# Performance work log

Measured on AMD Instinct MI355X. Metric: run time of the kernel, lower is better.

The kernel has to match this reference:

```python
import jax, jax.numpy as jnp
import numpy as np

B, T, N, PRED, DM = 16, 512, 128, 256, 32
L = T + PRED  # 768; conv windows 12 then 4: 768 -> 64 -> 16
EPS = 1e-5


def _conv1d(x, w, b, stride):
    # x: [B, C, L'], w: [C, C, k], kernel_size == stride, VALID (matches torch Conv1d)
    out = jax.lax.conv_general_dilated(x, w, (stride,), 'VALID',
                                       dimension_numbers=('NCH', 'OIH', 'NCH'))
    return out + b[None, :, None]


def _conv2d(x, w, b, pad):
    out = jax.lax.conv_general_dilated(x, w, (1, 1), [(pad, pad), (pad, pad)],
                                       dimension_numbers=('NCHW', 'OIHW', 'NCHW'))
    return out + b[None, :, None, None]


def _bn1d(x, g, b):
    # BatchNorm1d, training-mode batch statistics over (batch, length) per channel
    mu = x.mean((0, 2), keepdims=True)
    var = ((x - mu) ** 2).mean((0, 2), keepdims=True)
    return (x - mu) * jax.lax.rsqrt(var + EPS) * g[None, :, None] + b[None, :, None]


def _cubic_spline(y, size):
    # Natural cubic spline through values y: [B, Lk, C] at knots t = linspace(0,1,Lk),
    # evaluated at linspace(0,1,size). Natural BC: second derivative M=0 at endpoints.
    Bb, Lk, C = y.shape
    h = 1.0 / (Lk - 1)
    # tridiagonal system for interior second derivatives (uniform knots):
    # M[i-1] + 4 M[i] + M[i+1] = 6 * (y[i+1] - 2 y[i] + y[i-1]) / h^2
    m = Lk - 2
    rhs = (y[:, 2:, :] - 2.0 * y[:, 1:-1, :] + y[:, :-2, :]) * (6.0 / (h * h))  # [B,m,C]
    A = 4.0 * jnp.eye(m, dtype=y.dtype) + jnp.eye(m, k=1, dtype=y.dtype) + jnp.eye(m, k=-1, dtype=y.dtype)
    Mi = jnp.linalg.solve(A, rhs.transpose(1, 0, 2).reshape(m, Bb * C))  # [m, B*C]
    Mi = Mi.reshape(m, Bb, C).transpose(1, 0, 2)
    M = jnp.pad(Mi, ((0, 0), (1, 1), (0, 0)))  # [B, Lk, C], M[0]=M[-1]=0
    q = jnp.linspace(0.0, 1.0, size).astype(y.dtype)
    idx = jnp.clip(jnp.floor(q * (Lk - 1)).astype(jnp.int32), 0, Lk - 2)  # [size]
    s = (q - idx.astype(y.dtype) * h)[None, :, None]  # offset within interval
    u = h - s
    yi, yi1 = y[:, idx, :], y[:, idx + 1, :]
    M0, M1 = M[:, idx, :], M[:, idx + 1, :]
    hh6 = h * h / 6.0
    return ((M0 * u ** 3 + M1 * s ** 3) / (6.0 * h)
            + (yi - M0 * hh6) * (u / h)
            + (yi1 - M1 * hh6) * (s / h))  # [B, size, C]


def _forward(batch_x, le_w, le_b, c1_w, c1_b, bn1_g, bn1_b, c2_w, c2_b, bn2_g, bn2_b,
             i1_w0, i1_b0, i1_w1, i1_b1, i2_w0, i2_b0, i2_w1, i2_b1, ld_w, ld_b):
    # instance norm over time
    means = batch_x.mean(1, keepdims=True)
    xc = batch_x - means
    stdev = jnp.sqrt(xc.var(axis=1, keepdims=True) + EPS)
    xn = xc / stdev                               # [B, T, N]
    x = xn.transpose(0, 2, 1)                     # [B, N, T]
    x = jnp.einsum('bnt,lt->bnl', x, le_w) + le_b  # length_encoder -> [B, N, L]
    # multi-scale downsampling conv + spline back up to L
    scales = []
    t = x
    for win, cw, cb, g, bb in ((12, c1_w, c1_b, bn1_g, bn1_b), (4, c2_w, c2_b, bn2_g, bn2_b)):
        t = jax.nn.elu(_bn1d(_conv1d(t, cw, cb, win), g, bb))      # [B, N, L//...]
        scales.append(_cubic_spline(t.transpose(0, 2, 1), L).transpose(0, 2, 1))  # [B, N, L]
    a = jnp.stack([x] + scales, axis=1).transpose(0, 1, 3, 2)  # [B, 3, L, N]
    # Inception block 1 (num_kernels=2: 1x1 and 3x3, averaged), Dropout(eval)=id, GELU(exact)
    h1 = 0.5 * (_conv2d(a, i1_w0, i1_b0, 0) + _conv2d(a, i1_w1, i1_b1, 1))  # [B, DM, L, N]
    h1 = jax.nn.gelu(h1, approximate=False)
    # Inception block 2 -> 1 channel
    h2 = 0.5 * (_conv2d(h1, i2_w0, i2_b0, 0) + _conv2d(h1, i2_w1, i2_b1, 1))  # [B, 1, L, N]
    co = x + h2[:, 0].transpose(0, 2, 1)          # residual, [B, N, L]
    f = jnp.einsum('bnl,pl->bnp', co, ld_w) + ld_b  # length_decoder -> [B, N, PRED]
    f = f.transpose(0, 2, 1)                      # [B, PRED, N]
    return f * stdev[:, 0, :][:, None, :] + means[:, 0, :][:, None, :]


def setup_inputs():
    key = jax.random.key(0)
    ks = jax.random.split(key, 20)
    def w(i, shape, scale=0.02):
        return scale * jax.random.normal(ks[i], shape, jnp.float32)
    return dict(
        batch_x=jax.random.normal(ks[0], (B, T, N), jnp.float32),
        batch_x_mark=jax.random.normal(ks[1], (B, T, 4), jnp.float32),
        dec_inp=jax.random.normal(ks[2], (B, PRED, N), jnp.float32),
        batch_y_mark=jax.random.normal(ks[3], (B, PRED, 4), jnp.float32),
        le_w=w(4, (L, T)), le_b=w(5, (L,)),
        c1_w=w(6, (N, N, 12)), c1_b=w(7, (N,)),
        bn1_g=jnp.ones((N,), jnp.float32), bn1_b=jnp.zeros((N,), jnp.float32),
        c2_w=w(8, (N, N, 4)), c2_b=w(9, (N,)),
        bn2_g=jnp.ones((N,), jnp.float32), bn2_b=jnp.zeros((N,), jnp.float32),
        i1_w0=w(10, (DM, 3, 1, 1), 0.1), i1_b0=jnp.zeros((DM,), jnp.float32),
        i1_w1=w(11, (DM, 3, 3, 3), 0.1), i1_b1=jnp.zeros((DM,), jnp.float32),
        i2_w0=w(12, (1, DM, 1, 1), 0.1), i2_b0=jnp.zeros((1,), jnp.float32),
        i2_w1=w(13, (1, DM, 3, 3), 0.1), i2_b1=jnp.zeros((1,), jnp.float32),
        ld_w=w(14, (PRED, L)), ld_b=w(15, (PRED,)),
    )


def reference(batch_x, batch_x_mark, dec_inp, batch_y_mark, le_w, le_b,
              c1_w, c1_b, bn1_g, bn1_b, c2_w, c2_b, bn2_g, bn2_b,
              i1_w0, i1_b0, i1_w1, i1_b1, i2_w0, i2_b0, i2_w1, i2_b1, ld_w, ld_b):
    # batch_x_mark / dec_inp / batch_y_mark are accepted but unused (as in the torch forward)
    return _forward(batch_x, le_w, le_b, c1_w, c1_b, bn1_g, bn1_b, c2_w, c2_b, bn2_g, bn2_b,
                    i1_w0, i1_b0, i1_w1, i1_b1, i2_w0, i2_b0, i2_w1, i2_b1, ld_w, ld_b)
```

## Files before the change

### kernel.cpp

```cpp
#include <hip/hip_runtime.h>
#include <hip/hip_bf16.h>
#include <math.h>

#define BB 16
#define TT 512
#define NN 128
#define PREDN 256
#define DMC 32
#define LL 768
constexpr float EPSF = 1e-5f;
using bf16 = __hip_bfloat16;
using frag_ab = __attribute__((ext_vector_type(8))) short;
using frag_cd = __attribute__((ext_vector_type(4))) float;

__device__ __forceinline__ unsigned pbf2(float a, float b){
  union { bf16 h; unsigned short u; } x, y;
  x.h = __float2bfloat16(a); y.h = __float2bfloat16(b);
  return (unsigned)x.u | ((unsigned)y.u << 16);
}

__device__ __forceinline__ unsigned short bf16b(float v){
  union { bf16 h; unsigned short u; } x;
  x.h = __float2bfloat16(v);
  return x.u;
}

__device__ __forceinline__ float gelu_fast(float s){
  float s2v = s*s;
  float e = exp2f(s*fmaf(s2v, 0.10294396f, 2.30211806f));
  return s*e*__builtin_amdgcn_rcpf(e + 1.f);
}

__global__ void k_pre(const float* __restrict__ bx, const float* __restrict__ v0,
                      const float* __restrict__ v1, const float* __restrict__ w1c,
                      const float* __restrict__ w2c, float* __restrict__ sp,
                      float* __restrict__ s2p, float* __restrict__ vwsT,
                      float* __restrict__ wT1, float* __restrict__ wT2){
  int blk = blockIdx.x;
  if(blk < 64){
    int b = blk >> 2, tq = blk & 3, n = threadIdx.x;
    const float* p = bx + (size_t)b*TT*NN + (size_t)tq*128*NN + n;
    float s = 0.f, s2 = 0.f;
    for(int t=0;t<128;t++){ float v = p[(size_t)t*NN]; s += v; s2 += v*v; }
    sp[tq*2048 + b*NN + n] = s;
    s2p[tq*2048 + b*NN + n] = s2;
  } else if(blk == 64){
    for(int i=threadIdx.x; i<9*DMC; i+=blockDim.x){
      int tap = i/DMC, c = i%DMC;
      float wv = 0.5f*v1[c*9 + tap];
      if(tap == 4) wv += 0.5f*v0[c];
      vwsT[i] = wv;
    }
  } else if(blk <= 192){
    int o = blk - 65;
    for(int k=threadIdx.x; k<1536; k+=blockDim.x)
      wT1[(size_t)k*NN + o] = w1c[(size_t)o*1536 + k];
  } else {
    int o = blk - 193;
    for(int k=threadIdx.x; k<512; k+=blockDim.x)
      wT2[(size_t)k*NN + o] = w2c[(size_t)o*512 + k];
  }
}

__global__ __launch_bounds__(256) void k_gemm1(const float* __restrict__ bx, const float* __restrict__ lew,
    const float* __restrict__ leb, const float* __restrict__ sp, const float* __restrict__ s2p,
    float* __restrict__ x, float* __restrict__ a0){
  __shared__ unsigned Asu[64*20];
  __shared__ unsigned Bsu[64*20];
  int tid = threadIdx.x;
  int row0 = blockIdx.x*64, l0 = blockIdx.y*64;
  int b = row0 >> 7, n0 = row0 & 127;
  int lane = tid & 63, wv = tid >> 6;
  frag_cd acc[4] = {};
  int an = tid & 63, akq = (tid >> 6)*8;
  float mu_a, rs_a;
  {
    int rowa = row0 + an;
    float ssum = 0.f, s2sum = 0.f;
    #pragma unroll
    for(int tq=0;tq<4;tq++){ ssum += sp[tq*2048 + rowa]; s2sum += s2p[tq*2048 + rowa]; }
    mu_a = ssum*(1.f/512.f);
    rs_a = 1.f/sqrtf(fmaxf(s2sum*(1.f/512.f) - mu_a*mu_a, 0.f) + EPSF);
  }
  int btk = tid & 15, blc = tid >> 4;
  unsigned ra[4], rbq[4];
  #pragma unroll
  for(int u=0;u<4;u++){
    float v0 = (bx[((size_t)b*TT + akq + 2*u)*NN + n0 + an] - mu_a)*rs_a;
    float v1 = (bx[((size_t)b*TT + akq + 2*u + 1)*NN + n0 + an] - mu_a)*rs_a;
    ra[u] = pbf2(v0, v1);
    const float* lp = lew + (size_t)(l0 + blc + 16*u)*TT + 2*btk;
    rbq[u] = pbf2(lp[0], lp[1]);
  }
  int fr = wv*16 + (lane & 15);
  int fq = (lane >> 4)*4;
  for(int k0=0;k0<TT;k0+=32){
    *(uint4*)&Asu[an*20 + (akq>>1)] = make_uint4(ra[0], ra[1], ra[2], ra[3]);
    #pragma unroll
    for(int p=0;p<4;p++) Bsu[(blc + 16*p)*20 + btk] = rbq[p];
    __syncthreads();
    if(k0 + 32 < TT){
      #pragma unroll
      for(int u=0;u<4;u++){
        float v0 = (bx[((size_t)b*TT + k0 + 32 + akq + 2*u)*NN + n0 + an] - mu_a)*rs_a;
        float v1 = (bx[((size_t)b*TT + k0 + 32 + akq + 2*u + 1)*NN + n0 + an] - mu_a)*rs_a;
        ra[u] = pbf2(v0, v1);
        const float* lp = lew + (size_t)(l0 + blc + 16*u)*TT + k0 + 32 + 2*btk;
        rbq[u] = pbf2(lp[0], lp[1]);
      }
    }
    frag_ab af = *(const frag_ab*)&Asu[fr*20 + fq];
    #pragma unroll
    for(int nt=0;nt<4;nt++){
      frag_ab bf = *(const frag_ab*)&Bsu[(nt*16 + (lane & 15))*20 + fq];
      acc[nt] = __builtin_amdgcn_mfma_f32_16x16x32_bf16(af, bf, acc[nt], 0, 0, 0);
    }
    __syncthreads();
  }
  int col = lane & 15, quad = lane >> 4;
  #pragma unroll
  for(int nt=0;nt<4;nt++){
    int l = l0 + nt*16 + col;
    float lb = leb[l];
    #pragma unroll
    for(int r=0;r<4;r++){
      int m = wv*16 + quad*4 + r;
      x[(size_t)(row0 + m)*LL + l] = acc[nt][r] + lb;
    }
    float4 st;
    st.x = acc[nt][0] + lb;
    st.y = acc[nt][1] + lb;
    st.z = acc[nt][2] + lb;
    st.w = acc[nt][3] + lb;
    *(float4*)&a0[((size_t)b*LL + l)*NN + n0 + wv*16 + quad*4] = st;
  }
}

__global__ __launch_bounds__(512) void k_conv1(const float* __restrict__ x, const float* __restrict__ wT,
                                               const float* __restrict__ bias, float* __restrict__ t1){
  __shared__ alignas(16) float xs[NN*48];
  int jt = blockIdx.x, b = blockIdx.y;
  int tid = threadIdx.x;
  int o = tid & 127, jj = tid >> 7;
  for(int i=tid;i<NN*48;i+=512){
    int ci = i/48, kk = i%48;
    xs[i] = x[((size_t)b*NN + ci)*LL + jt*48 + kk];
  }
  __syncthreads();
  float a0 = 0.f, a1 = 0.f, a2 = 0.f, a3 = 0.f;
  for(int ci=0;ci<NN;ci++){
    const float* xc = xs + ci*48 + jj*12;
    const float* wc = wT + (size_t)(ci*12)*NN + o;
    #pragma unroll
    for(int kk=0;kk<12;kk+=4){
      a0 = fmaf(xc[kk+0], wc[(size_t)(kk+0)*NN], a0);
      a1 = fmaf(xc[kk+1], wc[(size_t)(kk+1)*NN], a1);
      a2 = fmaf(xc[kk+2], wc[(size_t)(kk+2)*NN], a2);
      a3 = fmaf(xc[kk+3], wc[(size_t)(kk+3)*NN], a3);
    }
  }
  int j = jt*4 + jj;
  t1[((size_t)b*NN + o)*64 + j] = (a0 + a1) + (a2 + a3) + bias[o];
}

__global__ void k_bnstats(const float* __restrict__ t, const float* __restrict__ g, const float* __restrict__ bb,
                          int Bcnt, int Jcnt, float* __restrict__ scale, float* __restrict__ shift){
  int o = blockIdx.x;
  int tot = Bcnt*Jcnt;
  float s = 0.f, s2 = 0.f;
  for(int i=threadIdx.x; i<tot; i+=blockDim.x){
    int b = i / Jcnt, j = i % Jcnt;
    float v = t[((size_t)b*NN + o)*Jcnt + j];
    s += v; s2 += v*v;
  }
  __shared__ float rs[256], rs2[256];
  rs[threadIdx.x] = s; rs2[threadIdx.x] = s2;
  __syncthreads();
  for(int st=128; st>0; st>>=1){
    if(threadIdx.x < st){ rs[threadIdx.x] += rs[threadIdx.x+st]; rs2[threadIdx.x] += rs2[threadIdx.x+st]; }
    __syncthreads();
  }
  if(threadIdx.x == 0){
    float mu = rs[0]/tot;
    float var = fmaxf(rs2[0]/tot - mu*mu, 0.f);
    float sc = g[o] * rsqrtf(var + EPSF);
    scale[o] = sc; shift[o] = bb[o] - mu*sc;
  }
}

__global__ void k_bnelu_t(const float* __restrict__ t, const float* __restrict__ scale,
                          const float* __restrict__ shift, int Jcnt, float* __restrict__ tt){
  int j = blockIdx.x, b = blockIdx.y, o = threadIdx.x;
  float v = t[((size_t)b*NN + o)*Jcnt + j]*scale[o] + shift[o];
  v = v > 0.f ? v : (expf(v) - 1.f);
  tt[((size_t)b*Jcnt + j)*NN + o] = v;
}

template<int LK>
__global__ void k_spline_solve(const float* __restrict__ y, float* __restrict__ M){
  constexpr int m = LK-2;
  const float Kc = 6.f*(LK-1)*(LK-1);
  __shared__ float cp[m];
  __shared__ float dp[m][NN];
  int b = blockIdx.x, c = threadIdx.x;
  if(c == 0){
    float cv = 0.25f; cp[0] = cv;
    for(int i=1;i<m;i++){ cv = 1.f/(4.f - cv); cp[i] = cv; }
  }
  __syncthreads();
  const float* yb = y + (size_t)b*LK*NN + c;
  float y0 = yb[0], y1 = yb[NN];
  float dprev = 0.f;
  for(int i=0;i<m;i++){
    float y2 = yb[(size_t)(i+2)*NN];
    float r = (y2 - 2.f*y1 + y0)*Kc;
    float d = (i == 0) ? r*0.25f : (r - dprev)*cp[i];
    dp[i][c] = d; dprev = d;
    y0 = y1; y1 = y2;
  }
  float* Mb = M + (size_t)b*LK*NN + c;
  float xv = dp[m-1][c];
  Mb[(size_t)m*NN] = xv;
  for(int i=m-2;i>=0;i--){
    xv = dp[i][c] - cp[i]*xv;
    Mb[(size_t)(i+1)*NN] = xv;
  }
  Mb[0] = 0.f;
  Mb[(size_t)(LK-1)*NN] = 0.f;
}

__device__ __forceinline__ float spline_pt(const float* __restrict__ y, const float* __restrict__ M,
                                           int LK, int l, int b, int c){
  float hh = 1.f/(LK-1);
  float q = (float)l * (1.f/(LL-1));
  int idx = (int)floorf(q*(LK-1));
  if(idx > LK-2) idx = LK-2;
  float s = q - idx*hh;
  float u = hh - s;
  const float* yb = y + ((size_t)b*LK + idx)*NN + c;
  const float* Mb = M + ((size_t)b*LK + idx)*NN + c;
  float yi = yb[0], yi1 = yb[NN], M0 = Mb[0], M1 = Mb[NN];
  float hh6 = hh*hh/6.f;
  return (M0*u*u*u + M1*s*s*s)*(1.f/(6.f*hh))
       + (yi  - M0*hh6)*(u*(1.f/hh))
       + (yi1 - M1*hh6)*(s*(1.f/hh));
}

__global__ __launch_bounds__(512) void k_conv2(const float* __restrict__ tt, const float* __restrict__ wT,
                                               const float* __restrict__ bias, float* __restrict__ t2){
  __shared__ alignas(16) float ts[16*NN];
  int jt = blockIdx.x, b = blockIdx.y;
  int tid = threadIdx.x;
  int o = tid & 127, jj = tid >> 7;
  for(int i=tid;i<16*NN;i+=512)
    ts[i] = tt[((size_t)b*64 + jt*16)*NN + i];
  __syncthreads();
  float a0 = 0.f, a1 = 0.f, a2 = 0.f, a3 = 0.f;
  for(int ci=0;ci<NN;ci++){
    const float* wc = wT + (size_t)(ci*4)*NN + o;
    const float* tc2 = ts + (jj*4)*NN + ci;
    a0 = fmaf(tc2[0*NN], wc[0*NN], a0);
    a1 = fmaf(tc2[1*NN], wc[1*NN], a1);
    a2 = fmaf(tc2[2*NN], wc[2*NN], a2);
    a3 = fmaf(tc2[3*NN], wc[3*NN], a3);
  }
  int j = jt*4 + jj;
  t2[((size_t)b*NN + o)*16 + j] = (a0 + a1) + (a2 + a3) + bias[o];
}

constexpr int KOFF[27] = {
    0,   1,   2,  36,  37,  38,  72,  73,  74,
  432, 433, 434, 468, 469, 470, 504, 505, 506,
  864, 865, 866, 900, 901, 902, 936, 937, 938
};

#define PBQ 1416
__global__ __launch_bounds__(256, 5) void k_h12(const float* __restrict__ a0,
    const float* __restrict__ y64, const float* __restrict__ M64,
    const float* __restrict__ y16, const float* __restrict__ M16,
    const float* __restrict__ w0, const float* __restrict__ b0,
    const float* __restrict__ w1, const float* __restrict__ b1,
    const float* __restrict__ vwsT, const float* __restrict__ vb0,
    const float* __restrict__ vb1, float* __restrict__ co){
  constexpr int AR = 12, AC = 36;
  __shared__ alignas(16) float as[3][AR][AC];
  __shared__ alignas(16) unsigned Au[4*PBQ];
  int tid = threadIdx.x;
  int l0 = blockIdx.x*8, n0 = blockIdx.y*32, b = blockIdx.z;
  int lane = tid & 63, wv = tid >> 6;

  float* asf = &as[0][0][0];
  for(int i=tid; i<3*AR*AC; i+=256){
    int ch = i/(AR*AC), rem = i%(AR*AC), yy = rem/AC, xx = rem%AC;
    int gl = l0 + yy - 2, gn = n0 + xx - 2;
    float v = 0.f;
    if(gl >= 0 && gl < LL && gn >= 0 && gn < NN){
      if(ch == 0)      v = a0[((size_t)b*LL + gl)*NN + gn];
      else if(ch == 1) v = spline_pt(y64, M64, 64, gl, b, gn);
      else             v = spline_pt(y16, M16, 16, gl, b, gn);
    }
    asf[i] = v;
  }

  int colB = lane & 15, kq = (lane >> 4)*8;
  union { uint4 q; frag_ab f; } bw0, bw1;
  {
    float w8[2][8];
    #pragma unroll
    for(int nt=0;nt<2;nt++){
      #pragma unroll
      for(int j=0;j<8;j++){
        int k = kq + j;
        float w = 0.f;
        if(k < 27){
          int ci = k/9, r9 = k - ci*9, dy = r9/3, dx = r9 - dy*3;
          int c = nt*16 + colB;
          w = 0.5f*w1[((c*3+ci)*3+dy)*3+dx];
          if(dy==1 && dx==1) w += 0.5f*w0[c*3+ci];
        }
        w8[nt][j] = w;
      }
    }
    bw0.q = make_uint4(pbf2(w8[0][0],w8[0][1]), pbf2(w8[0][2],w8[0][3]),
                       pbf2(w8[0][4],w8[0][5]), pbf2(w8[0][6],w8[0][7]));
    bw1.q = make_uint4(pbf2(w8[1][0],w8[1][1]), pbf2(w8[1][2],w8[1][3]),
                       pbf2(w8[1][4],w8[1][5]), pbf2(w8[1][6],w8[1][7]));
  }
  float br0 = 0.5f*(b0[colB] + b1[colB]);
  float br1 = 0.5f*(b0[16 + colB] + b1[16 + colB]);
  __syncthreads();

  for(int base=0; base<352; base+=128){
    int px = base + (tid >> 1);
    int half = tid & 1;
    if(px < 352){
      uint4 oA, oB;
      if(px < 340){
        int yy = px/34, xx = px - yy*34;
        const float* bp = asf + yy*AC + xx;
        if(half == 0){
          oA.x = pbf2(bp[KOFF[0]],  bp[KOFF[1]]);
          oA.y = pbf2(bp[KOFF[2]],  bp[KOFF[3]]);
          oA.z = pbf2(bp[KOFF[4]],  bp[KOFF[5]]);
          oA.w = pbf2(bp[KOFF[6]],  bp[KOFF[7]]);
          oB.x = pbf2(bp[KOFF[8]],  bp[KOFF[9]]);
          oB.y = pbf2(bp[KOFF[10]], bp[KOFF[11]]);
          oB.z = pbf2(bp[KOFF[12]], bp[KOFF[13]]);
          oB.w = pbf2(bp[KOFF[14]], bp[KOFF[15]]);
        } else {
          oA.x = pbf2(bp[KOFF[16]], bp[KOFF[17]]);
          oA.y = pbf2(bp[KOFF[18]], bp[KOFF[19]]);
          oA.z = pbf2(bp[KOFF[20]], bp[KOFF[21]]);
          oA.w = pbf2(bp[KOFF[22]], bp[KOFF[23]]);
          oB.x = pbf2(bp[KOFF[24]], bp[KOFF[25]]);
          oB.y = pbf2(bp[KOFF[26]], 0.f);
          oB.z = 0u; oB.w = 0u;
        }
      } else {
        oA = make_uint4(0u,0u,0u,0u);
        oB = make_uint4(0u,0u,0u,0u);
      }
      *(uint4*)&Au[(2*half)*PBQ + px*4]     = oA;
      *(uint4*)&Au[(2*half+1)*PBQ + px*4]   = oB;
    }
  }
  __syncthreads();

  unsigned short* h1h = (unsigned short*)Au;
  frag_cd zac = {0.f, 0.f, 0.f, 0.f};
  int qg = lane >> 4;
  int g0 = colB >> 3, s0 = colB & 7;
  for(int t = wv; t < 22; t += 4){
    int arow = t*16 + colB;
    union { uint4 q; frag_ab f; } av;
    av.q = *(const uint4*)&Au[qg*PBQ + arow*4];
    frag_cd d0 = __builtin_amdgcn_mfma_f32_16x16x32_bf16(av.f, bw0.f, zac, 0, 0, 0);
    frag_cd d1 = __builtin_amdgcn_mfma_f32_16x16x32_bf16(av.f, bw1.f, zac, 0, 0, 0);
    int px0 = t*16 + qg*4;
    #pragma unroll
    for(int r=0;r<4;r++){
      int px = px0 + r;
      h1h[(g0*PBQ + px*4)*2 + s0]     = bf16b(gelu_fast(d0[r] + br0));
      h1h[((g0+2)*PBQ + px*4)*2 + s0] = bf16b(gelu_fast(d1[r] + br1));
    }
  }
  __syncthreads();

  if(n0 == 0){
    for(int i=tid;i<10*32;i+=256){ int yy=i>>5, ch=i&31;
      h1h[((ch>>3)*PBQ + (yy*34)*4)*2 + (ch&7)] = 0; }
  }
  if(n0 == 96){
    for(int i=tid;i<10*32;i+=256){ int yy=i>>5, ch=i&31;
      h1h[((ch>>3)*PBQ + (yy*34+33)*4)*2 + (ch&7)] = 0; }
  }
  if(l0 == 0){
    for(int i=tid;i<34*32;i+=256){ int xx=i>>5, ch=i&31;
      h1h[((ch>>3)*PBQ + xx*4)*2 + (ch&7)] = 0; }
  }
  if(l0 == 760){
    for(int i=tid;i<34*32;i+=256){ int xx=i>>5, ch=i&31;
      h1h[((ch>>3)*PBQ + (9*34+xx)*4)*2 + (ch&7)] = 0; }
  }

  union { uint4 q; frag_ab f; } aw[9];
  {
    bool wlane = (lane & 15) == 0;
    int c8 = qg*8;
    #pragma unroll
    for(int tap=0; tap<9; tap++){
      const float* wp = vwsT + tap*DMC + c8;
      float4 wa = *(const float4*)wp;
      float4 wb = *(const float4*)(wp+4);
      if(!wlane){ wa = make_float4(0.f,0.f,0.f,0.f); wb = make_float4(0.f,0.f,0.f,0.f); }
      aw[tap].q = make_uint4(pbf2(wa.x,wa.y), pbf2(wa.z,wa.w), pbf2(wb.x,wb.y), pbf2(wb.z,wb.w));
    }
  }
  float vbsum = vb0[0] + vb1[0];
  __syncthreads();

  frag_cd cacc[4] = {};
  int baseoff[4];
  #pragma unroll
  for(int tt=0; tt<4; tt++){
    int px = (wv*4 + tt)*16 + (lane & 15);
    int yy = px >> 5, xx = px & 31;
    baseoff[tt] = qg*PBQ + (yy*34 + xx)*4;
  }
  #pragma unroll
  for(int dy=0; dy<3; dy++)
    #pragma unroll
    for(int dx=0; dx<3; dx++){
      int tap = dy*3 + dx;
      int off = (dy*34 + dx)*4;
      #pragma unroll
      for(int tt=0; tt<4; tt++){
        union { uint4 q; frag_ab f; } bv;
        bv.q = *(const uint4*)&Au[baseoff[tt] + off];
        cacc[tt] = __builtin_amdgcn_mfma_f32_16x16x32_bf16(aw[tap].f, bv.f, cacc[tt], 0, 0, 0);
      }
    }
  if(lane < 16){
    #pragma unroll
    for(int tt=0; tt<4; tt++){
      int px = (wv*4 + tt)*16 + lane;
      int yy = px >> 5, xx = px & 31;
      float res = as[0][yy+2][xx+2];
      size_t idx = ((size_t)b*LL + l0 + yy)*NN + n0 + xx;
      co[idx] = cacc[tt][0] + vbsum + res;
    }
  }
}

__global__ __launch_bounds__(256) void k_gemm2(const float* __restrict__ a0, const float* __restrict__ ldw,
    const float* __restrict__ ldb, const float* __restrict__ sp, const float* __restrict__ s2p,
    float* __restrict__ out){
  __shared__ unsigned Asu[64*20];
  __shared__ unsigned Bsu[32*20];
  int tid = threadIdx.x;
  int row0 = blockIdx.x*64, p0 = blockIdx.y*32;
  int b = row0 >> 7, n0 = row0 & 127;
  int lane = tid & 63, wv = tid >> 6;
  frag_cd acc[2] = {};
  int an = tid & 63, akq = (tid >> 6)*8;
  int btk = tid & 15, blc = tid >> 4;
  unsigned ra[4], rbq[2];
  #pragma unroll
  for(int u=0;u<4;u++){
    float v0 = a0[((size_t)b*LL + akq + 2*u)*NN + n0 + an];
    float v1 = a0[((size_t)b*LL + akq + 2*u + 1)*NN + n0 + an];
    ra[u] = pbf2(v0, v1);
  }
  #pragma unroll
  for(int u=0;u<2;u++){
    const float* lp = ldw + (size_t)(p0 + blc + 16*u)*LL + 2*btk;
    rbq[u] = pbf2(lp[0], lp[1]);
  }
  int fr = wv*16 + (lane & 15);
  int fq = (lane >> 4)*4;
  for(int k0=0;k0<LL;k0+=32){
    *(uint4*)&Asu[an*20 + (akq>>1)] = make_uint4(ra[0], ra[1], ra[2], ra[3]);
    #pragma unroll
    for(int p=0;p<2;p++) Bsu[(blc + 16*p)*20 + btk] = rbq[p];
    __syncthreads();
    if(k0 + 32 < LL){
      #pragma unroll
      for(int u=0;u<4;u++){
        float v0 = a0[((size_t)b*LL + k0 + 32 + akq + 2*u)*NN + n0 + an];
        float v1 = a0[((size_t)b*LL + k0 + 32 + akq + 2*u + 1)*NN + n0 + an];
        ra[u] = pbf2(v0, v1);
      }
      #pragma unroll
      for(int u=0;u<2;u++){
        const float* lp = ldw + (size_t)(p0 + blc + 16*u)*LL + k0 + 32 + 2*btk;
        rbq[u] = pbf2(lp[0], lp[1]);
      }
    }
    frag_ab af = *(const frag_ab*)&Asu[fr*20 + fq];
    #pragma unroll
    for(int nt=0;nt<2;nt++){
      frag_ab bf = *(const frag_ab*)&Bsu[(nt*16 + (lane & 15))*20 + fq];
      acc[nt] = __builtin_amdgcn_mfma_f32_16x16x32_bf16(af, bf, acc[nt], 0, 0, 0);
    }
    __syncthreads();
  }
  int col = lane & 15, quad = lane >> 4;
  float mu_r[4], sd_r[4];
  #pragma unroll
  for(int r=0;r<4;r++){
    int row = row0 + wv*16 + quad*4 + r;
    float ssum = 0.f, s2sum = 0.f;
    #pragma unroll
    for(int tq=0;tq<4;tq++){ ssum += sp[tq*2048 + row]; s2sum += s2p[tq*2048 + row]; }
    float mu = ssum*(1.f/512.f);
    float var = fmaxf(s2sum*(1.f/512.f) - mu*mu, 0.f);
    mu_r[r] = mu; sd_r[r] = sqrtf(var + EPSF);
  }
  #pragma unroll
  for(int nt=0;nt<2;nt++){
    int p = p0 + nt*16 + col;
    float lb = ldb[p];
    float4 st;
    st.x = (acc[nt][0] + lb)*sd_r[0] + mu_r[0];
    st.y = (acc[nt][1] + lb)*sd_r[1] + mu_r[1];
    st.z = (acc[nt][2] + lb)*sd_r[2] + mu_r[2];
    st.w = (acc[nt][3] + lb)*sd_r[3] + mu_r[3];
    *(float4*)&out[((size_t)b*PREDN + p)*NN + n0 + wv*16 + quad*4] = st;
  }
}

extern "C" void kernel_launch(void* const* d_in, const int* in_sizes, int n_in,
                              void* d_out, int out_size, void* d_ws, size_t ws_size,
                              hipStream_t stream){
  (void)in_sizes; (void)n_in; (void)out_size; (void)ws_size;
  const float* batch_x = (const float*)d_in[0];
  const float* le_w  = (const float*)d_in[4];
  const float* le_b  = (const float*)d_in[5];
  const float* c1_w  = (const float*)d_in[6];
  const float* c1_b  = (const float*)d_in[7];
  const float* bn1_g = (const float*)d_in[8];
  const float* bn1_b = (const float*)d_in[9];
  const float* c2_w  = (const float*)d_in[10];
  const float* c2_b  = (const float*)d_in[11];
  const float* bn2_g = (const float*)d_in[12];
  const float* bn2_b = (const float*)d_in[13];
  const float* i1_w0 = (const float*)d_in[14];
  const float* i1_b0 = (const float*)d_in[15];
  const float* i1_w1 = (const float*)d_in[16];
  const float* i1_b1 = (const float*)d_in[17];
  const float* i2_w0 = (const float*)d_in[18];
  const float* i2_b0 = (const float*)d_in[19];
  const float* i2_w1 = (const float*)d_in[20];
  const float* i2_b1 = (const float*)d_in[21];
  const float* ld_w  = (const float*)d_in[22];
  const float* ld_b  = (const float*)d_in[23];
  float* out = (float*)d_out;

  float* ws   = (float*)d_ws;
  float* sp   = ws;
  float* s2p  = sp + 8192;
  float* vwsT = s2p + 8192;
  float* wT1  = vwsT + 320;
  float* wT2  = wT1 + 196608;
  float* x    = wT2 + 65536;
  float* a0   = x + (size_t)BB*NN*LL;
  float* t1   = a0 + (size_t)BB*LL*NN;
  float* t1t  = t1 + (size_t)BB*NN*64;
  float* sc1  = t1t + (size_t)BB*64*NN;
  float* sh1  = sc1 + NN;
  float* Msp1 = sh1 + NN;
  float* t2   = Msp1 + (size_t)BB*64*NN;
  float* t2t  = t2 + (size_t)BB*NN*16;
  float* sc2  = t2t + (size_t)BB*16*NN;
  float* sh2  = sc2 + NN;
  float* Msp2 = sh2 + NN;
  float* co   = Msp2 + (size_t)BB*16*NN;

  k_pre<<<321, 128, 0, stream>>>(batch_x, i2_w0, i2_w1, c1_w, c2_w, sp, s2p, vwsT, wT1, wT2);
  k_gemm1<<<dim3(32,12), 256, 0, stream>>>(batch_x, le_w, le_b, sp, s2p, x, a0);
  k_conv1<<<dim3(16,BB), 512, 0, stream>>>(x, wT1, c1_b, t1);
  k_bnstats<<<NN, 256, 0, stream>>>(t1, bn1_g, bn1_b, BB, 64, sc1, sh1);
  k_bnelu_t<<<dim3(64,BB), NN, 0, stream>>>(t1, sc1, sh1, 64, t1t);
  k_spline_solve<64><<<BB, NN, 0, stream>>>(t1t, Msp1);
  k_conv2<<<dim3(4,BB), 512, 0, stream>>>(t1t, wT2, c2_b, t2);
  k_bnstats<<<NN, 256, 0, stream>>>(t2, bn2_g, bn2_b, BB, 16, sc2, sh2);
  k_bnelu_t<<<dim3(16,BB), NN, 0, stream>>>(t2, sc2, sh2, 16, t2t);
  k_spline_solve<16><<<BB, NN, 0, stream>>>(t2t, Msp2);
  k_h12<<<dim3(96,4,BB), 256, 0, stream>>>(a0, t1t, Msp1, t2t, Msp2,
                                           i1_w0, i1_b0, i1_w1, i1_b1,
                                           vwsT, i2_b0, i2_b1, co);
  k_gemm2<<<dim3(32,8), 256, 0, stream>>>(co, ld_w, ld_b, sp, s2p, out);
}
```

Before: 299.6 us.

## Pre-convert GEMM operands to bf16 and prepack conv weights in setup kernel

Adds a normalization-stats kernel and a kernel that writes normalized batch_x as bf16. k_pre gains blocks that pre-convert le_w and ld_w to packed bf16 and pre-pack the inception conv weights and summed biases. k_h12 now stages its input tile in shared memory as bf16, reorders its MFMA operands for vectorized output stores, and writes its result as bf16 for k_gemm2. This is meant to halve global traffic in the GEMMs and remove repeated per-block weight conversion, at the cost of two extra launches and an extra bf16 rounding point on the residual output.

```diff
diff --git a/kernel.cpp b/kernel.cpp
--- a/kernel.cpp
+++ b/kernel.cpp
@@ -33,9 +33,15 @@
 
 __global__ void k_pre(const float* __restrict__ bx, const float* __restrict__ v0,
                       const float* __restrict__ v1, const float* __restrict__ w1c,
-                      const float* __restrict__ w2c, float* __restrict__ sp,
-                      float* __restrict__ s2p, float* __restrict__ vwsT,
-                      float* __restrict__ wT1, float* __restrict__ wT2){
+                      const float* __restrict__ w2c, const float* __restrict__ w0s1,
+                      const float* __restrict__ w1s1, const float* __restrict__ b0s1,
+                      const float* __restrict__ b1s1, const float* __restrict__ lew,
+                      const float* __restrict__ ldw,
+                      float* __restrict__ sp, float* __restrict__ s2p,
+                      float* __restrict__ wT1, float* __restrict__ wT2,
+                      uint4* __restrict__ bwpk, uint4* __restrict__ awpk,
+                      float* __restrict__ bsum, unsigned* __restrict__ lewbf,
+                      unsigned* __restrict__ ldwbf){
   int blk = blockIdx.x;
   if(blk < 64){
     int b = blk >> 2, tq = blk & 3, n = threadIdx.x;
@@ -44,26 +50,91 @@
     for(int t=0;t<128;t++){ float v = p[(size_t)t*NN]; s += v; s2 += v*v; }
     sp[tq*2048 + b*NN + n] = s;
     s2p[tq*2048 + b*NN + n] = s2;
-  } else if(blk == 64){
-    for(int i=threadIdx.x; i<9*DMC; i+=blockDim.x){
-      int tap = i/DMC, c = i%DMC;
-      float wv = 0.5f*v1[c*9 + tap];
-      if(tap == 4) wv += 0.5f*v0[c];
-      vwsT[i] = wv;
-    }
-  } else if(blk <= 192){
-    int o = blk - 65;
+  } else if(blk < 192){
+    int o = blk - 64;
     for(int k=threadIdx.x; k<1536; k+=blockDim.x)
       wT1[(size_t)k*NN + o] = w1c[(size_t)o*1536 + k];
-  } else {
-    int o = blk - 193;
+  } else if(blk < 320){
+    int o = blk - 192;
     for(int k=threadIdx.x; k<512; k+=blockDim.x)
       wT2[(size_t)k*NN + o] = w2c[(size_t)o*512 + k];
-  }
-}
-
-__global__ __launch_bounds__(256) void k_gemm1(const float* __restrict__ bx, const float* __restrict__ lew,
-    const float* __restrict__ leb, const float* __restrict__ sp, const float* __restrict__ s2p,
+  } else if(blk == 320){
+    int i = threadIdx.x;
+    {
+      int c = i >> 2, kq = i & 3;
+      float w8[8];
+      #pragma unroll
+      for(int j=0;j<8;j++){
+        int k = kq*8+j; float w = 0.f;
+        if(k < 27){
+          int ci = k/9, r9 = k - ci*9, dy = r9/3, dx = r9 - dy*3;
+          w = 0.5f*w1s1[((c*3+ci)*3+dy)*3+dx];
+          if(dy==1 && dx==1) w += 0.5f*w0s1[c*3+ci];
+        }
+        w8[j] = w;
+      }
+      bwpk[i] = make_uint4(pbf2(w8[0],w8[1]), pbf2(w8[2],w8[3]),
+                           pbf2(w8[4],w8[5]), pbf2(w8[6],w8[7]));
+    }
+    if(i < 36){
+      int tap = i >> 2, qq = i & 3, c8 = qq*8;
+      float w8[8];
+      #pragma unroll
+      for(int j=0;j<8;j++){
+        int c = c8 + j;
+        w8[j] = 0.5f*v1[c*9 + tap] + ((tap==4) ? 0.5f*v0[c] : 0.f);
+      }
+      awpk[i] = make_uint4(pbf2(w8[0],w8[1]), pbf2(w8[2],w8[3]),
+                           pbf2(w8[4],w8[5]), pbf2(w8[6],w8[7]));
+    }
+    if(i < 32) bsum[i] = 0.5f*(b0s1[i] + b1s1[i]);
+  } else if(blk < 449){
+    int o = blk - 321;
+    for(int i=threadIdx.x; i<1536; i+=128){
+      int l = o*6 + i/256, tp = i%256;
+      lewbf[(size_t)l*256 + tp] = pbf2(lew[(size_t)l*TT + 2*tp], lew[(size_t)l*TT + 2*tp + 1]);
+    }
+  } else {
+    int o = blk - 449;
+    for(int i=threadIdx.x; i<1536; i+=128){
+      int p = o*4 + i/384, tp = i%384;
+      ldwbf[(size_t)p*384 + tp] = pbf2(ldw[(size_t)p*LL + 2*tp], ldw[(size_t)p*LL + 2*tp + 1]);
+    }
+  }
+}
+
+__global__ void k_musd(const float* __restrict__ sp, const float* __restrict__ s2p,
+                       float* __restrict__ mu, float* __restrict__ rs){
+  int i = blockIdx.x*256 + threadIdx.x;
+  float ss = 0.f, s2 = 0.f;
+  #pragma unroll
+  for(int tq=0;tq<4;tq++){ ss += sp[tq*2048 + i]; s2 += s2p[tq*2048 + i]; }
+  float m = ss*(1.f/512.f);
+  mu[i] = m;
+  rs[i] = 1.f/sqrtf(fmaxf(s2*(1.f/512.f) - m*m, 0.f) + EPSF);
+}
+
+__global__ __launch_bounds__(256) void k_xbf(const float* __restrict__ bx, const float* __restrict__ mu,
+                                             const float* __restrict__ rs, unsigned short* __restrict__ xbf){
+  int idx = blockIdx.x*256 + threadIdx.x;
+  int ng = idx & 15, t = (idx >> 4) & 511, b = idx >> 13;
+  int n8 = ng*8;
+  const float* p = bx + ((size_t)b*TT + t)*NN + n8;
+  float4 va = *(const float4*)p, vb2 = *(const float4*)(p+4);
+  const float* mp = mu + b*NN + n8;
+  const float* rp = rs + b*NN + n8;
+  float4 m0 = *(const float4*)mp, m1 = *(const float4*)(mp+4);
+  float4 r0 = *(const float4*)rp, r1 = *(const float4*)(rp+4);
+  uint4 o;
+  o.x = pbf2((va.x - m0.x)*r0.x, (va.y - m0.y)*r0.y);
+  o.y = pbf2((va.z - m0.z)*r0.z, (va.w - m0.w)*r0.w);
+  o.z = pbf2((vb2.x - m1.x)*r1.x, (vb2.y - m1.y)*r1.y);
+  o.w = pbf2((vb2.z - m1.z)*r1.z, (vb2.w - m1.w)*r1.w);
+  *(uint4*)&xbf[((size_t)b*TT + t)*NN + n8] = o;
+}
+
+__global__ __launch_bounds__(256) void k_gemm1(const unsigned short* __restrict__ xbf,
+    const unsigned* __restrict__ lewbf, const float* __restrict__ leb,
     float* __restrict__ x, float* __restrict__ a0){
   __shared__ unsigned Asu[64*20];
   __shared__ unsigned Bsu[64*20];
@@ -73,24 +144,14 @@
   int lane = tid & 63, wv = tid >> 6;
   frag_cd acc[4] = {};
   int an = tid & 63, akq = (tid >> 6)*8;
-  float mu_a, rs_a;
-  {
-    int rowa = row0 + an;
-    float ssum = 0.f, s2sum = 0.f;
-    #pragma unroll
-    for(int tq=0;tq<4;tq++){ ssum += sp[tq*2048 + rowa]; s2sum += s2p[tq*2048 + rowa]; }
-    mu_a = ssum*(1.f/512.f);
-    rs_a = 1.f/sqrtf(fmaxf(s2sum*(1.f/512.f) - mu_a*mu_a, 0.f) + EPSF);
-  }
   int btk = tid & 15, blc = tid >> 4;
   unsigned ra[4], rbq[4];
   #pragma unroll
   for(int u=0;u<4;u++){
-    float v0 = (bx[((size_t)b*TT + akq + 2*u)*NN + n0 + an] - mu_a)*rs_a;
-    float v1 = (bx[((size_t)b*TT + akq + 2*u + 1)*NN + n0 + an] - mu_a)*rs_a;
-    ra[u] = pbf2(v0, v1);
-    const float* lp = lew + (size_t)(l0 + blc + 16*u)*TT + 2*btk;
-    rbq[u] = pbf2(lp[0], lp[1]);
+    unsigned lo = xbf[((size_t)b*TT + akq + 2*u)*NN + n0 + an];
+    unsigned hi = xbf[((size_t)b*TT + akq + 2*u + 1)*NN + n0 + an];
+    ra[u] = lo | (hi << 16);
+    rbq[u] = lewbf[(size_t)(l0 + blc + 16*u)*256 + btk];
   }
   int fr = wv*16 + (lane & 15);
   int fq = (lane >> 4)*4;
@@ -102,11 +163,10 @@
     if(k0 + 32 < TT){
       #pragma unroll
       for(int u=0;u<4;u++){
-        float v0 = (bx[((size_t)b*TT + k0 + 32 + akq + 2*u)*NN + n0 + an] - mu_a)*rs_a;
-        float v1 = (bx[((size_t)b*TT + k0 + 32 + akq + 2*u + 1)*NN + n0 + an] - mu_a)*rs_a;
-        ra[u] = pbf2(v0, v1);
-        const float* lp = lew + (size_t)(l0 + blc + 16*u)*TT + k0 + 32 + 2*btk;
-        rbq[u] = pbf2(lp[0], lp[1]);
+        unsigned lo = xbf[((size_t)b*TT + k0 + 32 + akq + 2*u)*NN + n0 + an];
+        unsigned hi = xbf[((size_t)b*TT + k0 + 32 + akq + 2*u + 1)*NN + n0 + an];
+        ra[u] = lo | (hi << 16);
+        rbq[u] = lewbf[(size_t)(l0 + blc + 16*u)*256 + ((k0 + 32) >> 1) + btk];
       }
     }
     frag_ab af = *(const frag_ab*)&Asu[fr*20 + fq];
@@ -278,111 +338,89 @@
 __global__ __launch_bounds__(256, 5) void k_h12(const float* __restrict__ a0,
     const float* __restrict__ y64, const float* __restrict__ M64,
     const float* __restrict__ y16, const float* __restrict__ M16,
-    const float* __restrict__ w0, const float* __restrict__ b0,
-    const float* __restrict__ w1, const float* __restrict__ b1,
-    const float* __restrict__ vwsT, const float* __restrict__ vb0,
-    const float* __restrict__ vb1, float* __restrict__ co){
-  constexpr int AR = 12, AC = 36;
-  __shared__ alignas(16) float as[3][AR][AC];
+    const uint4* __restrict__ bwpk, const uint4* __restrict__ awpk,
+    const float* __restrict__ bsum, const float* __restrict__ vb0,
+    const float* __restrict__ vb1, unsigned short* __restrict__ cobf){
+  __shared__ alignas(16) unsigned short AsBf[3*12*36];
   __shared__ alignas(16) unsigned Au[4*PBQ];
   int tid = threadIdx.x;
   int l0 = blockIdx.x*8, n0 = blockIdx.y*32, b = blockIdx.z;
   int lane = tid & 63, wv = tid >> 6;
-
-  float* asf = &as[0][0][0];
-  for(int i=tid; i<3*AR*AC; i+=256){
-    int ch = i/(AR*AC), rem = i%(AR*AC), yy = rem/AC, xx = rem%AC;
-    int gl = l0 + yy - 2, gn = n0 + xx - 2;
-    float v = 0.f;
-    if(gl >= 0 && gl < LL && gn >= 0 && gn < NN){
-      if(ch == 0)      v = a0[((size_t)b*LL + gl)*NN + gn];
-      else if(ch == 1) v = spline_pt(y64, M64, 64, gl, b, gn);
-      else             v = spline_pt(y16, M16, 16, gl, b, gn);
-    }
-    asf[i] = v;
-  }
-
-  int colB = lane & 15, kq = (lane >> 4)*8;
-  union { uint4 q; frag_ab f; } bw0, bw1;
-  {
-    float w8[2][8];
-    #pragma unroll
-    for(int nt=0;nt<2;nt++){
-      #pragma unroll
-      for(int j=0;j<8;j++){
-        int k = kq + j;
-        float w = 0.f;
-        if(k < 27){
-          int ci = k/9, r9 = k - ci*9, dy = r9/3, dx = r9 - dy*3;
-          int c = nt*16 + colB;
-          w = 0.5f*w1[((c*3+ci)*3+dy)*3+dx];
-          if(dy==1 && dx==1) w += 0.5f*w0[c*3+ci];
-        }
-        w8[nt][j] = w;
+  int colB = lane & 15, qg = lane >> 4;
+
+  for(int i=tid; i<648; i+=256){
+    int ch = i/216, rem = i%216, yy = rem/18, xxp = rem%18;
+    int xx = xxp*2;
+    int gl = l0 + yy - 2, gn0 = n0 + xx - 2;
+    float v0 = 0.f, v1 = 0.f;
+    if(gl >= 0 && gl < LL){
+      if(ch == 0){
+        if((unsigned)gn0 < (unsigned)NN)     v0 = a0[((size_t)b*LL + gl)*NN + gn0];
+        if((unsigned)(gn0+1) < (unsigned)NN) v1 = a0[((size_t)b*LL + gl)*NN + gn0 + 1];
+      } else if(ch == 1){
+        if((unsigned)gn0 < (unsigned)NN)     v0 = spline_pt(y64, M64, 64, gl, b, gn0);
+        if((unsigned)(gn0+1) < (unsigned)NN) v1 = spline_pt(y64, M64, 64, gl, b, gn0+1);
+      } else {
+        if((unsigned)gn0 < (unsigned)NN)     v0 = spline_pt(y16, M16, 16, gl, b, gn0);
+        if((unsigned)(gn0+1) < (unsigned)NN) v1 = spline_pt(y16, M16, 16, gl, b, gn0+1);
       }
     }
-    bw0.q = make_uint4(pbf2(w8[0][0],w8[0][1]), pbf2(w8[0][2],w8[0][3]),
-                       pbf2(w8[0][4],w8[0][5]), pbf2(w8[0][6],w8[0][7]));
-    bw1.q = make_uint4(pbf2(w8[1][0],w8[1][1]), pbf2(w8[1][2],w8[1][3]),
-                       pbf2(w8[1][4],w8[1][5]), pbf2(w8[1][6],w8[1][7]));
-  }
-  float br0 = 0.5f*(b0[colB] + b1[colB]);
-  float br1 = 0.5f*(b0[16 + colB] + b1[16 + colB]);
+    *(unsigned*)&AsBf[i*2] = pbf2(v0, v1);
+  }
+
+  union U4 { uint4 q; frag_ab f; };
+  U4 bw0, bw1;
+  bw0.q = bwpk[colB*4 + qg];
+  bw1.q = bwpk[(colB + 16)*4 + qg];
+  float brA[4], brB[4];
+  #pragma unroll
+  for(int r=0;r<4;r++){ brA[r] = bsum[qg*4 + r]; brB[r] = bsum[16 + qg*4 + r]; }
   __syncthreads();
 
   for(int base=0; base<352; base+=128){
     int px = base + (tid >> 1);
     int half = tid & 1;
     if(px < 352){
-      uint4 oA, oB;
+      uint4 oA = make_uint4(0u,0u,0u,0u), oB = make_uint4(0u,0u,0u,0u);
       if(px < 340){
         int yy = px/34, xx = px - yy*34;
-        const float* bp = asf + yy*AC + xx;
+        const unsigned short* bp = AsBf + yy*36 + xx;
         if(half == 0){
-          oA.x = pbf2(bp[KOFF[0]],  bp[KOFF[1]]);
-          oA.y = pbf2(bp[KOFF[2]],  bp[KOFF[3]]);
-          oA.z = pbf2(bp[KOFF[4]],  bp[KOFF[5]]);
-          oA.w = pbf2(bp[KOFF[6]],  bp[KOFF[7]]);
-          oB.x = pbf2(bp[KOFF[8]],  bp[KOFF[9]]);
-          oB.y = pbf2(bp[KOFF[10]], bp[KOFF[11]]);
-          oB.z = pbf2(bp[KOFF[12]], bp[KOFF[13]]);
-          oB.w = pbf2(bp[KOFF[14]], bp[KOFF[15]]);
+          unsigned t0=bp[KOFF[0]],  t1=bp[KOFF[1]],  t2=bp[KOFF[2]],  t3=bp[KOFF[3]];
+          unsigned t4=bp[KOFF[4]],  t5=bp[KOFF[5]],  t6=bp[KOFF[6]],  t7=bp[KOFF[7]];
+          unsigned t8=bp[KOFF[8]],  t9=bp[KOFF[9]],  ta=bp[KOFF[10]], tb=bp[KOFF[11]];
+          unsigned tc=bp[KOFF[12]], td=bp[KOFF[13]], te=bp[KOFF[14]], tf=bp[KOFF[15]];
+          oA.x = t0 | (t1<<16); oA.y = t2 | (t3<<16); oA.z = t4 | (t5<<16); oA.w = t6 | (t7<<16);
+          oB.x = t8 | (t9<<16); oB.y = ta | (tb<<16); oB.z = tc | (td<<16); oB.w = te | (tf<<16);
         } else {
-          oA.x = pbf2(bp[KOFF[16]], bp[KOFF[17]]);
-          oA.y = pbf2(bp[KOFF[18]], bp[KOFF[19]]);
-          oA.z = pbf2(bp[KOFF[20]], bp[KOFF[21]]);
-          oA.w = pbf2(bp[KOFF[22]], bp[KOFF[23]]);
-          oB.x = pbf2(bp[KOFF[24]], bp[KOFF[25]]);
-          oB.y = pbf2(bp[KOFF[26]], 0.f);
-          oB.z = 0u; oB.w = 0u;
+          unsigned t0=bp[KOFF[16]], t1=bp[KOFF[17]], t2=bp[KOFF[18]], t3=bp[KOFF[19]];
+          unsigned t4=bp[KOFF[20]], t5=bp[KOFF[21]], t6=bp[KOFF[22]], t7=bp[KOFF[23]];
+          unsigned t8=bp[KOFF[24]], t9=bp[KOFF[25]], ta=bp[KOFF[26]];
+          oA.x = t0 | (t1<<16); oA.y = t2 | (t3<<16); oA.z = t4 | (t5<<16); oA.w = t6 | (t7<<16);
+          oB.x = t8 | (t9<<16); oB.y = ta;
         }
-      } else {
-        oA = make_uint4(0u,0u,0u,0u);
-        oB = make_uint4(0u,0u,0u,0u);
       }
-      *(uint4*)&Au[(2*half)*PBQ + px*4]     = oA;
-      *(uint4*)&Au[(2*half+1)*PBQ + px*4]   = oB;
+      *(uint4*)&Au[(2*half)*PBQ + px*4]   = oA;
+      *(uint4*)&Au[(2*half+1)*PBQ + px*4] = oB;
     }
   }
   __syncthreads();
 
   unsigned short* h1h = (unsigned short*)Au;
   frag_cd zac = {0.f, 0.f, 0.f, 0.f};
-  int qg = lane >> 4;
-  int g0 = colB >> 3, s0 = colB & 7;
   for(int t = wv; t < 22; t += 4){
-    int arow = t*16 + colB;
-    union { uint4 q; frag_ab f; } av;
-    av.q = *(const uint4*)&Au[qg*PBQ + arow*4];
-    frag_cd d0 = __builtin_amdgcn_mfma_f32_16x16x32_bf16(av.f, bw0.f, zac, 0, 0, 0);
-    frag_cd d1 = __builtin_amdgcn_mfma_f32_16x16x32_bf16(av.f, bw1.f, zac, 0, 0, 0);
-    int px0 = t*16 + qg*4;
-    #pragma unroll
-    for(int r=0;r<4;r++){
-      int px = px0 + r;
-      h1h[(g0*PBQ + px*4)*2 + s0]     = bf16b(gelu_fast(d0[r] + br0));
-      h1h[((g0+2)*PBQ + px*4)*2 + s0] = bf16b(gelu_fast(d1[r] + br1));
-    }
+    int px = t*16 + colB;
+    U4 av;
+    av.q = *(const uint4*)&Au[qg*PBQ + px*4];
+    frag_cd d0 = __builtin_amdgcn_mfma_f32_16x16x32_bf16(bw0.f, av.f, zac, 0, 0, 0);
+    frag_cd d1 = __builtin_amdgcn_mfma_f32_16x16x32_bf16(bw1.f, av.f, zac, 0, 0, 0);
+    unsigned u0 = pbf2(gelu_fast(d0[0] + brA[0]), gelu_fast(d0[1] + brA[1]));
+    unsigned u1 = pbf2(gelu_fast(d0[2] + brA[2]), gelu_fast(d0[3] + brA[3]));
+    unsigned u2 = pbf2(gelu_fast(d1[0] + brB[0]), gelu_fast(d1[1] + brB[1]));
+    unsigned u3 = pbf2(gelu_fast(d1[2] + brB[2]), gelu_fast(d1[3] + brB[3]));
+    int lo = (qg >> 1)*PBQ + px*4 + (qg & 1)*2;
+    *(uint2*)&Au[lo]           = make_uint2(u0, u1);
+    *(uint2*)&Au[2*PBQ + lo]   = make_uint2(u2, u3);
   }
   __syncthreads();
 
@@ -403,19 +441,9 @@
       h1h[((ch>>3)*PBQ + (9*34+xx)*4)*2 + (ch&7)] = 0; }
   }
 
-  union { uint4 q; frag_ab f; } aw[9];
-  {
-    bool wlane = (lane & 15) == 0;
-    int c8 = qg*8;
-    #pragma unroll
-    for(int tap=0; tap<9; tap++){
-      const float* wp = vwsT + tap*DMC + c8;
-      float4 wa = *(const float4*)wp;
-      float4 wb = *(const float4*)(wp+4);
-      if(!wlane){ wa = make_float4(0.f,0.f,0.f,0.f); wb = make_float4(0.f,0.f,0.f,0.f); }
-      aw[tap].q = make_uint4(pbf2(wa.x,wa.y), pbf2(wa.z,wa.w), pbf2(wb.x,wb.y), pbf2(wb.z,wb.w));
-    }
-  }
+  U4 aw[9];
+  #pragma unroll
+  for(int tap=0; tap<9; tap++) aw[tap].q = awpk[tap*4 + qg];
   float vbsum = vb0[0] + vb1[0];
   __syncthreads();
 
@@ -423,7 +451,7 @@
   int baseoff[4];
   #pragma unroll
   for(int tt=0; tt<4; tt++){
-    int px = (wv*4 + tt)*16 + (lane & 15);
+    int px = (wv*4 + tt)*16 + colB;
     int yy = px >> 5, xx = px & 31;
     baseoff[tt] = qg*PBQ + (yy*34 + xx)*4;
   }
@@ -435,7 +463,7 @@
       int off = (dy*34 + dx)*4;
       #pragma unroll
       for(int tt=0; tt<4; tt++){
-        union { uint4 q; frag_ab f; } bv;
+        U4 bv;
         bv.q = *(const uint4*)&Au[baseoff[tt] + off];
         cacc[tt] = __builtin_amdgcn_mfma_f32_16x16x32_bf16(aw[tap].f, bv.f, cacc[tt], 0, 0, 0);
       }
@@ -445,15 +473,15 @@
     for(int tt=0; tt<4; tt++){
       int px = (wv*4 + tt)*16 + lane;
       int yy = px >> 5, xx = px & 31;
-      float res = as[0][yy+2][xx+2];
       size_t idx = ((size_t)b*LL + l0 + yy)*NN + n0 + xx;
-      co[idx] = cacc[tt][0] + vbsum + res;
-    }
-  }
-}
-
-__global__ __launch_bounds__(256) void k_gemm2(const float* __restrict__ a0, const float* __restrict__ ldw,
-    const float* __restrict__ ldb, const float* __restrict__ sp, const float* __restrict__ s2p,
+      cobf[idx] = bf16b(cacc[tt][0] + vbsum + a0[idx]);
+    }
+  }
+}
+
+__global__ __launch_bounds__(256) void k_gemm2(const unsigned short* __restrict__ cobf,
+    const unsigned* __restrict__ ldwbf, const float* __restrict__ ldb,
+    const float* __restrict__ sp, const float* __restrict__ s2p,
     float* __restrict__ out){
   __shared__ unsigned Asu[64*20];
   __shared__ unsigned Bsu[32*20];
@@ -467,15 +495,13 @@
   unsigned ra[4], rbq[2];
   #pragma unroll
   for(int u=0;u<4;u++){
-    float v0 = a0[((size_t)b*LL + akq + 2*u)*NN + n0 + an];
-    float v1 = a0[((size_t)b*LL + akq + 2*u + 1)*NN + n0 + an];
-    ra[u] = pbf2(v0, v1);
-  }
-  #pragma unroll
-  for(int u=0;u<2;u++){
-    const float* lp = ldw + (size_t)(p0 + blc + 16*u)*LL + 2*btk;
-    rbq[u] = pbf2(lp[0], lp[1]);
-  }
+    unsigned lo = cobf[((size_t)b*LL + akq + 2*u)*NN + n0 + an];
+    unsigned hi = cobf[((size_t)b*LL + akq + 2*u + 1)*NN + n0 + an];
+    ra[u] = lo | (hi << 16);
+  }
+  #pragma unroll
+  for(int u=0;u<2;u++)
+    rbq[u] = ldwbf[(size_t)(p0 + blc + 16*u)*384 + btk];
   int fr = wv*16 + (lane & 15);
   int fq = (lane >> 4)*4;
   for(int k0=0;k0<LL;k0+=32){
@@ -486,15 +512,13 @@
     if(k0 + 32 < LL){
       #pragma unroll
       for(int u=0;u<4;u++){
-        float v0 = a0[((size_t)b*LL + k0 + 32 + akq + 2*u)*NN + n0 + an];
-        float v1 = a0[((size_t)b*LL + k0 + 32 + akq + 2*u + 1)*NN + n0 + an];
-        ra[u] = pbf2(v0, v1);
+        unsigned lo = cobf[((size_t)b*LL + k0 + 32 + akq + 2*u)*NN + n0 + an];
+        unsigned hi = cobf[((size_t)b*LL + k0 + 32 + akq + 2*u + 1)*NN + n0 + an];
+        ra[u] = lo | (hi << 16);
       }
       #pragma unroll
-      for(int u=0;u<2;u++){
-        const float* lp = ldw + (size_t)(p0 + blc + 16*u)*LL + k0 + 32 + 2*btk;
-        rbq[u] = pbf2(lp[0], lp[1]);
-      }
+      for(int u=0;u<2;u++)
+        rbq[u] = ldwbf[(size_t)(p0 + blc + 16*u)*384 + ((k0 + 32) >> 1) + btk];
     }
     frag_ab af = *(const frag_ab*)&Asu[fr*20 + fq];
     #pragma unroll
@@ -559,8 +583,7 @@
   float* ws   = (float*)d_ws;
   float* sp   = ws;
   float* s2p  = sp + 8192;
-  float* vwsT = s2p + 8192;
-  float* wT1  = vwsT + 320;
+  float* wT1  = s2p + 8192;
   float* wT2  = wT1 + 196608;
   float* x    = wT2 + 65536;
   float* a0   = x + (size_t)BB*NN*LL;
@@ -574,10 +597,29 @@
   float* sc2  = t2t + (size_t)BB*16*NN;
   float* sh2  = sc2 + NN;
   float* Msp2 = sh2 + NN;
-  float* co   = Msp2 + (size_t)BB*16*NN;
-
-  k_pre<<<321, 128, 0, stream>>>(batch_x, i2_w0, i2_w1, c1_w, c2_w, sp, s2p, vwsT, wT1, wT2);
-  k_gemm1<<<dim3(32,12), 256, 0, stream>>>(batch_x, le_w, le_b, sp, s2p, x, a0);
+  float* muv  = Msp2 + (size_t)BB*16*NN;
+  float* rsv  = muv + 2048;
+  float* fB1  = rsv + 2048;
+  unsigned short* xbf = (unsigned short*)fB1;
+  float* fB2  = fB1 + 524288;
+  unsigned* lewbf = (unsigned*)fB2;
+  float* fB3  = fB2 + 196608;
+  unsigned* ldwbf = (unsigned*)fB3;
+  float* fB4  = fB3 + 98304;
+  uint4* bwpk = (uint4*)fB4;
+  float* fB5  = fB4 + 512;
+  uint4* awpk = (uint4*)fB5;
+  float* fB6  = fB5 + 144;
+  float* bsum = fB6;
+  float* fB7  = fB6 + 32;
+  unsigned short* cobf = (unsigned short*)fB7;
+
+  k_pre<<<513, 128, 0, stream>>>(batch_x, i2_w0, i2_w1, c1_w, c2_w,
+                                 i1_w0, i1_w1, i1_b0, i1_b1, le_w, ld_w,
+                                 sp, s2p, wT1, wT2, bwpk, awpk, bsum, lewbf, ldwbf);
+  k_musd<<<8, 256, 0, stream>>>(sp, s2p, muv, rsv);
+  k_xbf<<<512, 256, 0, stream>>>(batch_x, muv, rsv, xbf);
+  k_gemm1<<<dim3(32,12), 256, 0, stream>>>(xbf, lewbf, le_b, x, a0);
   k_conv1<<<dim3(16,BB), 512, 0, stream>>>(x, wT1, c1_b, t1);
   k_bnstats<<<NN, 256, 0, stream>>>(t1, bn1_g, bn1_b, BB, 64, sc1, sh1);
   k_bnelu_t<<<dim3(64,BB), NN, 0, stream>>>(t1, sc1, sh1, 64, t1t);
@@ -587,7 +629,6 @@
   k_bnelu_t<<<dim3(16,BB), NN, 0, stream>>>(t2, sc2, sh2, 16, t2t);
   k_spline_solve<16><<<BB, NN, 0, stream>>>(t2t, Msp2);
   k_h12<<<dim3(96,4,BB), 256, 0, stream>>>(a0, t1t, Msp1, t2t, Msp2,
-                                           i1_w0, i1_b0, i1_w1, i1_b1,
-                                           vwsT, i2_b0, i2_b1, co);
-  k_gemm2<<<dim3(32,8), 256, 0, stream>>>(co, ld_w, ld_b, sp, s2p, out);
-}
+                                           bwpk, awpk, bsum, i2_b0, i2_b1, cobf);
+  k_gemm2<<<dim3(32,8), 256, 0, stream>>>(cobf, ldwbf, ld_b, sp, s2p, out);
+}
```

New measurement: 266.6 us. 11.0% less time.
